# Kernel optimization log

Hardware: AMD Instinct MI355X
Metric: run time of the kernel (lower is better)

Reference implementation:

```python
import jax, jax.numpy as jnp
import numpy as np


def setup_inputs() -> dict:
    key = jax.random.key(0)
    k1, k2, k3, k4 = jax.random.split(key, 4)
    B, S, D, R = 8, 1024, 1024, 256
    batch = jax.random.normal(k1, (B, S, D), dtype=jnp.float32)
    proj_L = jax.random.uniform(k2, (D, R), dtype=jnp.float32, minval=-0.05, maxval=0.05)
    proj_R = jax.random.uniform(k3, (R, D), dtype=jnp.float32, minval=-0.05, maxval=0.05)
    bias = jax.random.uniform(k4, (1,), dtype=jnp.float32, minval=-0.05, maxval=0.05)
    return {"batch": batch, "proj_L": proj_L, "proj_R": proj_R, "bias": bias}


def reference(batch, proj_L, proj_R, bias):
    # logits[b,i,j] = h_i^T (L @ R) h_j + bias
    # Efficient factored form (same math, avoids O(B*S^2*D) intermediates):
    # left[b,i,r] = (batch @ L)[b,i,r]; right[b,j,r] = (batch @ R^T)[b,j,r]
    left = jnp.einsum('bid,dr->bir', batch, proj_L)    # (B,S,R)
    right = jnp.einsum('bjd,rd->bjr', batch, proj_R)   # (B,S,R)
    logits = jnp.einsum('bir,bjr->bij', left, right) + bias[0]
    return logits
```

## Files before the change

kernel.cpp:

```cpp
#include <hip/hip_runtime.h>

typedef __bf16 bf16_t;
typedef __bf16 bf16x8 __attribute__((ext_vector_type(8)));
typedef __bf16 bf16x4 __attribute__((ext_vector_type(4)));
typedef float f32x4 __attribute__((ext_vector_type(4)));

__device__ __forceinline__ void async16(const void* g, void* l) {
  __builtin_amdgcn_global_load_lds(
      (const __attribute__((address_space(1))) unsigned int*)g,
      (__attribute__((address_space(3))) unsigned int*)l,
      16, 0, 0);
}

__global__ void prep_Bcat(const float* __restrict__ projL,
                          const float* __restrict__ projR,
                          bf16_t* __restrict__ Bcat) {
  const int t = threadIdx.x;
  if (blockIdx.x < 256) {
    int i = blockIdx.x * 256 + t;
    float4 v = ((const float4*)projR)[i];
    bf16x4 o;
    o[0] = (bf16_t)v.x; o[1] = (bf16_t)v.y; o[2] = (bf16_t)v.z; o[3] = (bf16_t)v.w;
    ((bf16x4*)(Bcat + (long)256 * 1024))[i] = o;
  } else {
    __shared__ float tile[32][33];
    const int bb = blockIdx.x - 256;
    const int n0 = (bb & 7) * 32;
    const int k0 = (bb >> 3) * 32;
    const int tx = t & 31;
    const int ty = t >> 5;
#pragma unroll
    for (int i = 0; i < 32; i += 8)
      tile[ty + i][tx] = projL[(long)(k0 + ty + i) * 256 + n0 + tx];
    __syncthreads();
#pragma unroll
    for (int i = 0; i < 32; i += 8)
      Bcat[(long)(n0 + ty + i) * 1024 + k0 + tx] = (bf16_t)tile[tx][ty + i];
  }
}

__global__ __launch_bounds__(256, 2) void gemm1_fusedA(
    const float* __restrict__ batch, const bf16_t* __restrict__ Bcat,
    bf16_t* __restrict__ LR) {
  const int bx = blockIdx.x;
  const int tm = (bx & 127) * 64;
  const int tn = (bx >> 7) * 128;

  __shared__ __attribute__((aligned(16))) bf16_t As[4 * 2048];
  __shared__ __attribute__((aligned(16))) bf16_t Bs[4 * 4096];

  const int t = threadIdx.x;
  const int lane = t & 63;
  const int quad = lane >> 4;
  const int l15 = lane & 15;
  const int wave = t >> 6;
  const int wr = (wave >> 1) * 32;
  const int wc = (wave & 1) * 64;

  const int rS = t >> 2;
  const int cS = (t & 3) * 8;
  const bf16_t* gB = Bcat + (long)(tn + rS) * 1024 + cS;
  bf16_t* lB = Bs + t * 8;

  const int rA = t >> 4;
  const int cA = (t & 15) * 8;
  const float* gA = batch + (long)(tm + rA) * 1024 + cA;
  bf16_t* lA = As + (cA >> 5) * 2048 + (cA & 31);

  f32x4 acc[2][4];
#pragma unroll
  for (int i = 0; i < 2; ++i)
#pragma unroll
    for (int j = 0; j < 4; ++j)
      acc[i][j] = (f32x4){0.f, 0.f, 0.f, 0.f};

  float4 fa[4], fb[4];
#pragma unroll
  for (int i = 0; i < 4; ++i) {
    const float* p = gA + (long)16 * i * 1024;
    fa[i] = *(const float4*)p;
    fb[i] = *(const float4*)(p + 4);
  }

  for (int s = 0; s < 8; ++s) {
    const int k0 = s * 128;
#pragma unroll
    for (int kc = 0; kc < 4; ++kc) {
      async16(gB + k0 + kc * 32, lB + kc * 4096);
      async16(gB + k0 + kc * 32 + (long)64 * 1024, lB + kc * 4096 + 2048);
    }
#pragma unroll
    for (int i = 0; i < 4; ++i) {
      bf16x8 v;
      v[0] = (bf16_t)fa[i].x; v[1] = (bf16_t)fa[i].y;
      v[2] = (bf16_t)fa[i].z; v[3] = (bf16_t)fa[i].w;
      v[4] = (bf16_t)fb[i].x; v[5] = (bf16_t)fb[i].y;
      v[6] = (bf16_t)fb[i].z; v[7] = (bf16_t)fb[i].w;
      *(bf16x8*)(lA + (rA + 16 * i) * 32) = v;
    }
    __syncthreads();

    if (s < 7) {
#pragma unroll
      for (int i = 0; i < 4; ++i) {
        const float* p = gA + (s + 1) * 128 + (long)16 * i * 1024;
        fa[i] = *(const float4*)p;
        fb[i] = *(const float4*)(p + 4);
      }
    }

#pragma unroll
    for (int kc = 0; kc < 4; ++kc) {
      const bf16_t* Ak = As + kc * 2048;
      const bf16_t* Bk = Bs + kc * 4096;
      bf16x8 af[2], bv[4];
#pragma unroll
      for (int i = 0; i < 2; ++i)
        af[i] = *(const bf16x8*)(Ak + (wr + i * 16 + l15) * 32 + quad * 8);
#pragma unroll
      for (int j = 0; j < 4; ++j)
        bv[j] = *(const bf16x8*)(Bk + (wc + j * 16 + l15) * 32 + quad * 8);
#pragma unroll
      for (int i = 0; i < 2; ++i)
#pragma unroll
        for (int j = 0; j < 4; ++j)
          acc[i][j] = __builtin_amdgcn_mfma_f32_16x16x32_bf16(af[i], bv[j],
                                                              acc[i][j], 0, 0, 0);
    }
    __syncthreads();
  }

#pragma unroll
  for (int i = 0; i < 2; ++i) {
    const int r0 = tm + wr + i * 16 + quad * 4;
#pragma unroll
    for (int j = 0; j < 4; ++j) {
      const int c0 = tn + wc + j * 16 + l15;
#pragma unroll
      for (int r = 0; r < 4; ++r)
        LR[(long)(r0 + r) * 512 + c0] = (bf16_t)acc[i][j][r];
    }
  }
}

__global__ __launch_bounds__(256, 2) void gemm2(const bf16_t* __restrict__ LR,
                                                float* __restrict__ out,
                                                const float* __restrict__ bias) {
  const int bx = blockIdx.x;
  const int bz = bx & 7;
  const int tile = bx >> 3;
  const int tm = (tile & 7) * 128;
  const int tn = (tile >> 3) * 128;
  const bf16_t* LRb = LR + (long)bz * 1024 * 512;

  __shared__ __attribute__((aligned(16))) bf16_t As[2 * 8192];
  __shared__ __attribute__((aligned(16))) bf16_t Bs[2 * 8192];

  const int t = threadIdx.x;
  const int lane = t & 63;
  const int quad = lane >> 4;
  const int l15 = lane & 15;
  const int wave = t >> 6;
  const int wr = (wave >> 1) * 64;
  const int wc = (wave & 1) * 64;

  const int rS = t >> 2;
  const int cS = (t & 3) * 8;
  const bf16_t* gA = LRb + (long)(tm + rS) * 512 + cS;
  const bf16_t* gB = LRb + (long)(tn + rS) * 512 + 256 + cS;

  f32x4 acc[4][4];
#pragma unroll
  for (int i = 0; i < 4; ++i)
#pragma unroll
    for (int j = 0; j < 4; ++j)
      acc[i][j] = (f32x4){0.f, 0.f, 0.f, 0.f};

  auto STAGE = [&](int buf, int s) {
    const int k0 = s * 64;
    bf16_t* dA = As + buf * 8192 + t * 8;
    bf16_t* dB = Bs + buf * 8192 + t * 8;
#pragma unroll
    for (int kc = 0; kc < 2; ++kc) {
      const int ko = k0 + kc * 32;
      async16(gA + ko, dA + kc * 4096);
      async16(gA + ko + (long)64 * 512, dA + kc * 4096 + 2048);
      async16(gB + ko, dB + kc * 4096);
      async16(gB + ko + (long)64 * 512, dB + kc * 4096 + 2048);
    }
  };

  STAGE(0, 0);
  __syncthreads();

#pragma unroll
  for (int s = 0; s < 4; ++s) {
    if (s < 3) STAGE((s + 1) & 1, s + 1);
    const bf16_t* Ab = As + (s & 1) * 8192;
    const bf16_t* Bb = Bs + (s & 1) * 8192;
#pragma unroll
    for (int kc = 0; kc < 2; ++kc) {
      const bf16_t* Ak = Ab + kc * 4096;
      const bf16_t* Bk = Bb + kc * 4096;
      bf16x8 af[4], bv[4];
#pragma unroll
      for (int i = 0; i < 4; ++i)
        af[i] = *(const bf16x8*)(Ak + (wr + i * 16 + l15) * 32 + quad * 8);
#pragma unroll
      for (int j = 0; j < 4; ++j)
        bv[j] = *(const bf16x8*)(Bk + (wc + j * 16 + l15) * 32 + quad * 8);
#pragma unroll
      for (int i = 0; i < 4; ++i)
#pragma unroll
        for (int j = 0; j < 4; ++j)
          acc[i][j] = __builtin_amdgcn_mfma_f32_16x16x32_bf16(af[i], bv[j],
                                                              acc[i][j], 0, 0, 0);
    }
    if (s < 3) __syncthreads();
  }

  float* C = out + (long)bz * 1024 * 1024;
  const float bvadd = bias[0];
#pragma unroll
  for (int i = 0; i < 4; ++i) {
    const int r0 = tm + wr + i * 16 + quad * 4;
#pragma unroll
    for (int j = 0; j < 4; ++j) {
      const int c0 = tn + wc + j * 16 + l15;
#pragma unroll
      for (int r = 0; r < 4; ++r)
        C[(long)(r0 + r) * 1024 + c0] = acc[i][j][r] + bvadd;
    }
  }
}

extern "C" void kernel_launch(void* const* d_in, const int* in_sizes, int n_in,
                              void* d_out, int out_size, void* d_ws,
                              size_t ws_size, hipStream_t stream) {
  const float* batch = (const float*)d_in[0];
  const float* projL = (const float*)d_in[1];
  const float* projR = (const float*)d_in[2];
  const float* bias = (const float*)d_in[3];
  float* out = (float*)d_out;

  char* ws = (char*)d_ws;
  bf16_t* Bcat = (bf16_t*)ws;
  bf16_t* LR = (bf16_t*)(ws + (long)512 * 1024 * 2);

  prep_Bcat<<<512, 256, 0, stream>>>(projL, projR, Bcat);

  gemm1_fusedA<<<512, 256, 0, stream>>>(batch, Bcat, LR);

  gemm2<<<512, 256, 0, stream>>>(LR, out, bias);
}
```

Before: 110.1 us.

## Fuse three kernels into one cooperative kernel with grid-wide syncs

Merges the weight-prep, first GEMM and second GEMM kernels into a single cooperative launch that separates the phases with grid.sync(), sharing one 64KB LDS buffer across phases. The aim is to remove two kernel launch gaps and their tail effects. In exchange it needs all 512 blocks co-resident (2 per CU on 256 CUs). Every block also waits at each grid barrier, and the 64KB static LDS may limit occupancy in phases that previously used less.

```diff
diff --git a/kernel.cpp b/kernel.cpp
--- a/kernel.cpp
+++ b/kernel.cpp
@@ -1,4 +1,7 @@
 #include <hip/hip_runtime.h>
+#include <hip/hip_cooperative_groups.h>
+
+namespace cg = cooperative_groups;
 
 typedef __bf16 bf16_t;
 typedef __bf16 bf16x8 __attribute__((ext_vector_type(8)));
@@ -12,19 +15,30 @@
       16, 0, 0);
 }
 
-__global__ void prep_Bcat(const float* __restrict__ projL,
-                          const float* __restrict__ projR,
-                          bf16_t* __restrict__ Bcat) {
+__global__ __launch_bounds__(256, 2) void fused_all(
+    const float* __restrict__ batch, const float* __restrict__ projL,
+    const float* __restrict__ projR, const float* __restrict__ bias,
+    float* __restrict__ out, bf16_t* __restrict__ Bcat,
+    bf16_t* __restrict__ LR) {
+  __shared__ __attribute__((aligned(16))) char smem[65536];
+  cg::grid_group grid = cg::this_grid();
+
   const int t = threadIdx.x;
-  if (blockIdx.x < 256) {
-    int i = blockIdx.x * 256 + t;
+  const int bx = blockIdx.x;
+  const int lane = t & 63;
+  const int quad = lane >> 4;
+  const int l15 = lane & 15;
+  const int wave = t >> 6;
+
+  if (bx < 256) {
+    int i = bx * 256 + t;
     float4 v = ((const float4*)projR)[i];
     bf16x4 o;
     o[0] = (bf16_t)v.x; o[1] = (bf16_t)v.y; o[2] = (bf16_t)v.z; o[3] = (bf16_t)v.w;
     ((bf16x4*)(Bcat + (long)256 * 1024))[i] = o;
   } else {
-    __shared__ float tile[32][33];
-    const int bb = blockIdx.x - 256;
+    float(*tile)[33] = (float(*)[33])smem;
+    const int bb = bx - 256;
     const int n0 = (bb & 7) * 32;
     const int k0 = (bb >> 3) * 32;
     const int tx = t & 31;
@@ -37,199 +51,183 @@
     for (int i = 0; i < 32; i += 8)
       Bcat[(long)(n0 + ty + i) * 1024 + k0 + tx] = (bf16_t)tile[tx][ty + i];
   }
-}
-
-__global__ __launch_bounds__(256, 2) void gemm1_fusedA(
-    const float* __restrict__ batch, const bf16_t* __restrict__ Bcat,
-    bf16_t* __restrict__ LR) {
-  const int bx = blockIdx.x;
-  const int tm = (bx & 127) * 64;
-  const int tn = (bx >> 7) * 128;
-
-  __shared__ __attribute__((aligned(16))) bf16_t As[4 * 2048];
-  __shared__ __attribute__((aligned(16))) bf16_t Bs[4 * 4096];
-
-  const int t = threadIdx.x;
-  const int lane = t & 63;
-  const int quad = lane >> 4;
-  const int l15 = lane & 15;
-  const int wave = t >> 6;
-  const int wr = (wave >> 1) * 32;
-  const int wc = (wave & 1) * 64;
-
-  const int rS = t >> 2;
-  const int cS = (t & 3) * 8;
-  const bf16_t* gB = Bcat + (long)(tn + rS) * 1024 + cS;
-  bf16_t* lB = Bs + t * 8;
-
-  const int rA = t >> 4;
-  const int cA = (t & 15) * 8;
-  const float* gA = batch + (long)(tm + rA) * 1024 + cA;
-  bf16_t* lA = As + (cA >> 5) * 2048 + (cA & 31);
-
-  f32x4 acc[2][4];
-#pragma unroll
-  for (int i = 0; i < 2; ++i)
-#pragma unroll
-    for (int j = 0; j < 4; ++j)
-      acc[i][j] = (f32x4){0.f, 0.f, 0.f, 0.f};
-
-  float4 fa[4], fb[4];
-#pragma unroll
-  for (int i = 0; i < 4; ++i) {
-    const float* p = gA + (long)16 * i * 1024;
-    fa[i] = *(const float4*)p;
-    fb[i] = *(const float4*)(p + 4);
+
+  grid.sync();
+
+  {
+    bf16_t* As = (bf16_t*)smem;
+    bf16_t* Bs = (bf16_t*)(smem + 16384);
+    const int tm = (bx & 127) * 64;
+    const int tn = (bx >> 7) * 128;
+    const int wr = (wave >> 1) * 32;
+    const int wc = (wave & 1) * 64;
+
+    const int rS = t >> 2;
+    const int cS = (t & 3) * 8;
+    const bf16_t* gB = Bcat + (long)(tn + rS) * 1024 + cS;
+    bf16_t* lB = Bs + t * 8;
+
+    const int rA = t >> 4;
+    const int cA = (t & 15) * 8;
+    const float* gA = batch + (long)(tm + rA) * 1024 + cA;
+    bf16_t* lA = As + (cA >> 5) * 2048 + (cA & 31);
+
+    f32x4 acc[2][4];
+#pragma unroll
+    for (int i = 0; i < 2; ++i)
+#pragma unroll
+      for (int j = 0; j < 4; ++j)
+        acc[i][j] = (f32x4){0.f, 0.f, 0.f, 0.f};
+
+    float4 fa[4], fb[4];
+#pragma unroll
+    for (int i = 0; i < 4; ++i) {
+      const float* p = gA + (long)16 * i * 1024;
+      fa[i] = *(const float4*)p;
+      fb[i] = *(const float4*)(p + 4);
+    }
+
+    for (int s = 0; s < 8; ++s) {
+      const int k0 = s * 128;
+#pragma unroll
+      for (int kc = 0; kc < 4; ++kc) {
+        async16(gB + k0 + kc * 32, lB + kc * 4096);
+        async16(gB + k0 + kc * 32 + (long)64 * 1024, lB + kc * 4096 + 2048);
+      }
+#pragma unroll
+      for (int i = 0; i < 4; ++i) {
+        bf16x8 v;
+        v[0] = (bf16_t)fa[i].x; v[1] = (bf16_t)fa[i].y;
+        v[2] = (bf16_t)fa[i].z; v[3] = (bf16_t)fa[i].w;
+        v[4] = (bf16_t)fb[i].x; v[5] = (bf16_t)fb[i].y;
+        v[6] = (bf16_t)fb[i].z; v[7] = (bf16_t)fb[i].w;
+        *(bf16x8*)(lA + (rA + 16 * i) * 32) = v;
+      }
+      __syncthreads();
+
+      if (s < 7) {
+#pragma unroll
+        for (int i = 0; i < 4; ++i) {
+          const float* p = gA + (s + 1) * 128 + (long)16 * i * 1024;
+          fa[i] = *(const float4*)p;
+          fb[i] = *(const float4*)(p + 4);
+        }
+      }
+
+#pragma unroll
+      for (int kc = 0; kc < 4; ++kc) {
+        const bf16_t* Ak = As + kc * 2048;
+        const bf16_t* Bk = Bs + kc * 4096;
+        bf16x8 af[2], bv[4];
+#pragma unroll
+        for (int i = 0; i < 2; ++i)
+          af[i] = *(const bf16x8*)(Ak + (wr + i * 16 + l15) * 32 + quad * 8);
+#pragma unroll
+        for (int j = 0; j < 4; ++j)
+          bv[j] = *(const bf16x8*)(Bk + (wc + j * 16 + l15) * 32 + quad * 8);
+#pragma unroll
+        for (int i = 0; i < 2; ++i)
+#pragma unroll
+          for (int j = 0; j < 4; ++j)
+            acc[i][j] = __builtin_amdgcn_mfma_f32_16x16x32_bf16(
+                af[i], bv[j], acc[i][j], 0, 0, 0);
+      }
+      __syncthreads();
+    }
+
+#pragma unroll
+    for (int i = 0; i < 2; ++i) {
+      const int r0 = tm + wr + i * 16 + quad * 4;
+#pragma unroll
+      for (int j = 0; j < 4; ++j) {
+        const int c0 = tn + wc + j * 16 + l15;
+#pragma unroll
+        for (int r = 0; r < 4; ++r)
+          LR[(long)(r0 + r) * 512 + c0] = (bf16_t)acc[i][j][r];
+      }
+    }
   }
 
-  for (int s = 0; s < 8; ++s) {
-    const int k0 = s * 128;
-#pragma unroll
-    for (int kc = 0; kc < 4; ++kc) {
-      async16(gB + k0 + kc * 32, lB + kc * 4096);
-      async16(gB + k0 + kc * 32 + (long)64 * 1024, lB + kc * 4096 + 2048);
-    }
+  grid.sync();
+
+  {
+    bf16_t* As = (bf16_t*)smem;
+    bf16_t* Bs = (bf16_t*)(smem + 32768);
+    const int bz = bx & 7;
+    const int tile = bx >> 3;
+    const int tm = (tile & 7) * 128;
+    const int tn = (tile >> 3) * 128;
+    const bf16_t* LRb = LR + (long)bz * 1024 * 512;
+    const int wr = (wave >> 1) * 64;
+    const int wc = (wave & 1) * 64;
+
+    const int rS = t >> 2;
+    const int cS = (t & 3) * 8;
+    const bf16_t* gA = LRb + (long)(tm + rS) * 512 + cS;
+    const bf16_t* gB = LRb + (long)(tn + rS) * 512 + 256 + cS;
+
+    f32x4 acc[4][4];
+#pragma unroll
+    for (int i = 0; i < 4; ++i)
+#pragma unroll
+      for (int j = 0; j < 4; ++j)
+        acc[i][j] = (f32x4){0.f, 0.f, 0.f, 0.f};
+
+    auto STAGE = [&](int buf, int s) {
+      const int k0 = s * 64;
+      bf16_t* dA = As + buf * 8192 + t * 8;
+      bf16_t* dB = Bs + buf * 8192 + t * 8;
+#pragma unroll
+      for (int kc = 0; kc < 2; ++kc) {
+        const int ko = k0 + kc * 32;
+        async16(gA + ko, dA + kc * 4096);
+        async16(gA + ko + (long)64 * 512, dA + kc * 4096 + 2048);
+        async16(gB + ko, dB + kc * 4096);
+        async16(gB + ko + (long)64 * 512, dB + kc * 4096 + 2048);
+      }
+    };
+
+    STAGE(0, 0);
+    __syncthreads();
+
+#pragma unroll
+    for (int s = 0; s < 4; ++s) {
+      if (s < 3) STAGE((s + 1) & 1, s + 1);
+      const bf16_t* Ab = As + (s & 1) * 8192;
+      const bf16_t* Bb = Bs + (s & 1) * 8192;
+#pragma unroll
+      for (int kc = 0; kc < 2; ++kc) {
+        const bf16_t* Ak = Ab + kc * 4096;
+        const bf16_t* Bk = Bb + kc * 4096;
+        bf16x8 af[4], bv[4];
+#pragma unroll
+        for (int i = 0; i < 4; ++i)
+          af[i] = *(const bf16x8*)(Ak + (wr + i * 16 + l15) * 32 + quad * 8);
+#pragma unroll
+        for (int j = 0; j < 4; ++j)
+          bv[j] = *(const bf16x8*)(Bk + (wc + j * 16 + l15) * 32 + quad * 8);
+#pragma unroll
+        for (int i = 0; i < 4; ++i)
+#pragma unroll
+          for (int j = 0; j < 4; ++j)
+            acc[i][j] = __builtin_amdgcn_mfma_f32_16x16x32_bf16(
+                af[i], bv[j], acc[i][j], 0, 0, 0);
+      }
+      if (s < 3) __syncthreads();
+    }
+
+    float* C = out + (long)bz * 1024 * 1024;
+    const float bvadd = bias[0];
 #pragma unroll
     for (int i = 0; i < 4; ++i) {
-      bf16x8 v;
-      v[0] = (bf16_t)fa[i].x; v[1] = (bf16_t)fa[i].y;
-      v[2] = (bf16_t)fa[i].z; v[3] = (bf16_t)fa[i].w;
-      v[4] = (bf16_t)fb[i].x; v[5] = (bf16_t)fb[i].y;
-      v[6] = (bf16_t)fb[i].z; v[7] = (bf16_t)fb[i].w;
-      *(bf16x8*)(lA + (rA + 16 * i) * 32) = v;
-    }
-    __syncthreads();
-
-    if (s < 7) {
-#pragma unroll
-      for (int i = 0; i < 4; ++i) {
-        const float* p = gA + (s + 1) * 128 + (long)16 * i * 1024;
-        fa[i] = *(const float4*)p;
-        fb[i] = *(const float4*)(p + 4);
-      }
-    }
-
-#pragma unroll
-    for (int kc = 0; kc < 4; ++kc) {
-      const bf16_t* Ak = As + kc * 2048;
-      const bf16_t* Bk = Bs + kc * 4096;
-      bf16x8 af[2], bv[4];
-#pragma unroll
-      for (int i = 0; i < 2; ++i)
-        af[i] = *(const bf16x8*)(Ak + (wr + i * 16 + l15) * 32 + quad * 8);
-#pragma unroll
-      for (int j = 0; j < 4; ++j)
-        bv[j] = *(const bf16x8*)(Bk + (wc + j * 16 + l15) * 32 + quad * 8);
-#pragma unroll
-      for (int i = 0; i < 2; ++i)
-#pragma unroll
-        for (int j = 0; j < 4; ++j)
-          acc[i][j] = __builtin_amdgcn_mfma_f32_16x16x32_bf16(af[i], bv[j],
-                                                              acc[i][j], 0, 0, 0);
-    }
-    __syncthreads();
-  }
-
-#pragma unroll
-  for (int i = 0; i < 2; ++i) {
-    const int r0 = tm + wr + i * 16 + quad * 4;
-#pragma unroll
-    for (int j = 0; j < 4; ++j) {
-      const int c0 = tn + wc + j * 16 + l15;
-#pragma unroll
-      for (int r = 0; r < 4; ++r)
-        LR[(long)(r0 + r) * 512 + c0] = (bf16_t)acc[i][j][r];
-    }
-  }
-}
-
-__global__ __launch_bounds__(256, 2) void gemm2(const bf16_t* __restrict__ LR,
-                                                float* __restrict__ out,
-                                                const float* __restrict__ bias) {
-  const int bx = blockIdx.x;
-  const int bz = bx & 7;
-  const int tile = bx >> 3;
-  const int tm = (tile & 7) * 128;
-  const int tn = (tile >> 3) * 128;
-  const bf16_t* LRb = LR + (long)bz * 1024 * 512;
-
-  __shared__ __attribute__((aligned(16))) bf16_t As[2 * 8192];
-  __shared__ __attribute__((aligned(16))) bf16_t Bs[2 * 8192];
-
-  const int t = threadIdx.x;
-  const int lane = t & 63;
-  const int quad = lane >> 4;
-  const int l15 = lane & 15;
-  const int wave = t >> 6;
-  const int wr = (wave >> 1) * 64;
-  const int wc = (wave & 1) * 64;
-
-  const int rS = t >> 2;
-  const int cS = (t & 3) * 8;
-  const bf16_t* gA = LRb + (long)(tm + rS) * 512 + cS;
-  const bf16_t* gB = LRb + (long)(tn + rS) * 512 + 256 + cS;
-
-  f32x4 acc[4][4];
-#pragma unroll
-  for (int i = 0; i < 4; ++i)
-#pragma unroll
-    for (int j = 0; j < 4; ++j)
-      acc[i][j] = (f32x4){0.f, 0.f, 0.f, 0.f};
-
-  auto STAGE = [&](int buf, int s) {
-    const int k0 = s * 64;
-    bf16_t* dA = As + buf * 8192 + t * 8;
-    bf16_t* dB = Bs + buf * 8192 + t * 8;
-#pragma unroll
-    for (int kc = 0; kc < 2; ++kc) {
-      const int ko = k0 + kc * 32;
-      async16(gA + ko, dA + kc * 4096);
-      async16(gA + ko + (long)64 * 512, dA + kc * 4096 + 2048);
-      async16(gB + ko, dB + kc * 4096);
-      async16(gB + ko + (long)64 * 512, dB + kc * 4096 + 2048);
-    }
-  };
-
-  STAGE(0, 0);
-  __syncthreads();
-
-#pragma unroll
-  for (int s = 0; s < 4; ++s) {
-    if (s < 3) STAGE((s + 1) & 1, s + 1);
-    const bf16_t* Ab = As + (s & 1) * 8192;
-    const bf16_t* Bb = Bs + (s & 1) * 8192;
-#pragma unroll
-    for (int kc = 0; kc < 2; ++kc) {
-      const bf16_t* Ak = Ab + kc * 4096;
-      const bf16_t* Bk = Bb + kc * 4096;
-      bf16x8 af[4], bv[4];
-#pragma unroll
-      for (int i = 0; i < 4; ++i)
-        af[i] = *(const bf16x8*)(Ak + (wr + i * 16 + l15) * 32 + quad * 8);
-#pragma unroll
-      for (int j = 0; j < 4; ++j)
-        bv[j] = *(const bf16x8*)(Bk + (wc + j * 16 + l15) * 32 + quad * 8);
-#pragma unroll
-      for (int i = 0; i < 4; ++i)
-#pragma unroll
-        for (int j = 0; j < 4; ++j)
-          acc[i][j] = __builtin_amdgcn_mfma_f32_16x16x32_bf16(af[i], bv[j],
-                                                              acc[i][j], 0, 0, 0);
-    }
-    if (s < 3) __syncthreads();
-  }
-
-  float* C = out + (long)bz * 1024 * 1024;
-  const float bvadd = bias[0];
-#pragma unroll
-  for (int i = 0; i < 4; ++i) {
-    const int r0 = tm + wr + i * 16 + quad * 4;
-#pragma unroll
-    for (int j = 0; j < 4; ++j) {
-      const int c0 = tn + wc + j * 16 + l15;
-#pragma unroll
-      for (int r = 0; r < 4; ++r)
-        C[(long)(r0 + r) * 1024 + c0] = acc[i][j][r] + bvadd;
+      const int r0 = tm + wr + i * 16 + quad * 4;
+#pragma unroll
+      for (int j = 0; j < 4; ++j) {
+        const int c0 = tn + wc + j * 16 + l15;
+#pragma unroll
+        for (int r = 0; r < 4; ++r)
+          C[(long)(r0 + r) * 1024 + c0] = acc[i][j][r] + bvadd;
+      }
     }
   }
 }
@@ -247,9 +245,8 @@
   bf16_t* Bcat = (bf16_t*)ws;
   bf16_t* LR = (bf16_t*)(ws + (long)512 * 1024 * 2);
 
-  prep_Bcat<<<512, 256, 0, stream>>>(projL, projR, Bcat);
-
-  gemm1_fusedA<<<512, 256, 0, stream>>>(batch, Bcat, LR);
-
-  gemm2<<<512, 256, 0, stream>>>(LR, out, bias);
+  void* args[] = {(void*)&batch, (void*)&projL, (void*)&projR, (void*)&bias,
+                  (void*)&out,   (void*)&Bcat,  (void*)&LR};
+  hipLaunchCooperativeKernel((void*)fused_all, dim3(512), dim3(256), args, 0,
+                             stream);
 }
```

Result: slower. 234.3 us (+112.8%).

## Double-buffer gemm1 K-loop and shrink gemm2 tiles to 64x64 for occupancy

Applied to the files above, without the earlier changes.

gemm1 now uses a 64-wide K step with double-buffered LDS for both A and B, prefetching the next stage's B asynchronously and converting A into the other buffer after the MFMAs. This leaves one barrier per step and lets loads overlap compute. gemm2 switches from 128x128 to 64x64 output tiles, 2048 blocks and a launch bound of 5 blocks per CU, to raise occupancy and wave count. The smaller tiles reload LR operands more often and do fewer MFMAs per LDS read.

```diff
diff --git a/kernel.cpp b/kernel.cpp
--- a/kernel.cpp
+++ b/kernel.cpp
@@ -46,8 +46,8 @@
   const int tm = (bx & 127) * 64;
   const int tn = (bx >> 7) * 128;
 
-  __shared__ __attribute__((aligned(16))) bf16_t As[4 * 2048];
-  __shared__ __attribute__((aligned(16))) bf16_t Bs[4 * 4096];
+  __shared__ __attribute__((aligned(16))) bf16_t As[2 * 4096];
+  __shared__ __attribute__((aligned(16))) bf16_t Bs[2 * 8192];
 
   const int t = threadIdx.x;
   const int lane = t & 63;
@@ -60,12 +60,10 @@
   const int rS = t >> 2;
   const int cS = (t & 3) * 8;
   const bf16_t* gB = Bcat + (long)(tn + rS) * 1024 + cS;
-  bf16_t* lB = Bs + t * 8;
-
-  const int rA = t >> 4;
-  const int cA = (t & 15) * 8;
+
+  const int rA = t >> 3;
+  const int cA = (t & 7) * 8;
   const float* gA = batch + (long)(tm + rA) * 1024 + cA;
-  bf16_t* lA = As + (cA >> 5) * 2048 + (cA & 31);
 
   f32x4 acc[2][4];
 #pragma unroll
@@ -74,45 +72,51 @@
     for (int j = 0; j < 4; ++j)
       acc[i][j] = (f32x4){0.f, 0.f, 0.f, 0.f};
 
-  float4 fa[4], fb[4];
-#pragma unroll
-  for (int i = 0; i < 4; ++i) {
-    const float* p = gA + (long)16 * i * 1024;
+  float4 fa[2], fb[2];
+#pragma unroll
+  for (int i = 0; i < 2; ++i) {
+    const float* p = gA + (long)32 * i * 1024;
     fa[i] = *(const float4*)p;
     fb[i] = *(const float4*)(p + 4);
   }
-
-  for (int s = 0; s < 8; ++s) {
-    const int k0 = s * 128;
-#pragma unroll
-    for (int kc = 0; kc < 4; ++kc) {
-      async16(gB + k0 + kc * 32, lB + kc * 4096);
-      async16(gB + k0 + kc * 32 + (long)64 * 1024, lB + kc * 4096 + 2048);
-    }
-#pragma unroll
-    for (int i = 0; i < 4; ++i) {
-      bf16x8 v;
-      v[0] = (bf16_t)fa[i].x; v[1] = (bf16_t)fa[i].y;
-      v[2] = (bf16_t)fa[i].z; v[3] = (bf16_t)fa[i].w;
-      v[4] = (bf16_t)fb[i].x; v[5] = (bf16_t)fb[i].y;
-      v[6] = (bf16_t)fb[i].z; v[7] = (bf16_t)fb[i].w;
-      *(bf16x8*)(lA + (rA + 16 * i) * 32) = v;
-    }
-    __syncthreads();
-
-    if (s < 7) {
-#pragma unroll
-      for (int i = 0; i < 4; ++i) {
-        const float* p = gA + (s + 1) * 128 + (long)16 * i * 1024;
+#pragma unroll
+  for (int kc = 0; kc < 2; ++kc) {
+    async16(gB + kc * 32, Bs + kc * 4096 + t * 8);
+    async16(gB + kc * 32 + (long)64 * 1024, Bs + kc * 4096 + 2048 + t * 8);
+  }
+#pragma unroll
+  for (int i = 0; i < 2; ++i) {
+    bf16x8 v;
+    v[0] = (bf16_t)fa[i].x; v[1] = (bf16_t)fa[i].y;
+    v[2] = (bf16_t)fa[i].z; v[3] = (bf16_t)fa[i].w;
+    v[4] = (bf16_t)fb[i].x; v[5] = (bf16_t)fb[i].y;
+    v[6] = (bf16_t)fb[i].z; v[7] = (bf16_t)fb[i].w;
+    *(bf16x8*)(As + (cA >> 5) * 2048 + (rA + 32 * i) * 32 + (cA & 31)) = v;
+  }
+  __syncthreads();
+
+  for (int s = 0; s < 16; ++s) {
+    const int buf = s & 1;
+    const int nb = buf ^ 1;
+    if (s < 15) {
+      const int k1 = (s + 1) * 64;
+#pragma unroll
+      for (int i = 0; i < 2; ++i) {
+        const float* p = gA + k1 + (long)32 * i * 1024;
         fa[i] = *(const float4*)p;
         fb[i] = *(const float4*)(p + 4);
       }
-    }
-
-#pragma unroll
-    for (int kc = 0; kc < 4; ++kc) {
-      const bf16_t* Ak = As + kc * 2048;
-      const bf16_t* Bk = Bs + kc * 4096;
+#pragma unroll
+      for (int kc = 0; kc < 2; ++kc) {
+        async16(gB + k1 + kc * 32, Bs + nb * 8192 + kc * 4096 + t * 8);
+        async16(gB + k1 + kc * 32 + (long)64 * 1024,
+                Bs + nb * 8192 + kc * 4096 + 2048 + t * 8);
+      }
+    }
+#pragma unroll
+    for (int kc = 0; kc < 2; ++kc) {
+      const bf16_t* Ak = As + buf * 4096 + kc * 2048;
+      const bf16_t* Bk = Bs + buf * 8192 + kc * 4096;
       bf16x8 af[2], bv[4];
 #pragma unroll
       for (int i = 0; i < 2; ++i)
@@ -127,7 +131,19 @@
           acc[i][j] = __builtin_amdgcn_mfma_f32_16x16x32_bf16(af[i], bv[j],
                                                               acc[i][j], 0, 0, 0);
     }
-    __syncthreads();
+    if (s < 15) {
+#pragma unroll
+      for (int i = 0; i < 2; ++i) {
+        bf16x8 v;
+        v[0] = (bf16_t)fa[i].x; v[1] = (bf16_t)fa[i].y;
+        v[2] = (bf16_t)fa[i].z; v[3] = (bf16_t)fa[i].w;
+        v[4] = (bf16_t)fb[i].x; v[5] = (bf16_t)fb[i].y;
+        v[6] = (bf16_t)fb[i].z; v[7] = (bf16_t)fb[i].w;
+        *(bf16x8*)(As + nb * 4096 + (cA >> 5) * 2048 + (rA + 32 * i) * 32 +
+                   (cA & 31)) = v;
+      }
+      __syncthreads();
+    }
   }
 
 #pragma unroll
@@ -143,50 +159,48 @@
   }
 }
 
-__global__ __launch_bounds__(256, 2) void gemm2(const bf16_t* __restrict__ LR,
+__global__ __launch_bounds__(256, 5) void gemm2(const bf16_t* __restrict__ LR,
                                                 float* __restrict__ out,
                                                 const float* __restrict__ bias) {
   const int bx = blockIdx.x;
   const int bz = bx & 7;
   const int tile = bx >> 3;
-  const int tm = (tile & 7) * 128;
-  const int tn = (tile >> 3) * 128;
+  const int tm = (tile & 15) * 64;
+  const int tn = (tile >> 4) * 64;
   const bf16_t* LRb = LR + (long)bz * 1024 * 512;
 
-  __shared__ __attribute__((aligned(16))) bf16_t As[2 * 8192];
-  __shared__ __attribute__((aligned(16))) bf16_t Bs[2 * 8192];
+  __shared__ __attribute__((aligned(16))) bf16_t As[2 * 4096];
+  __shared__ __attribute__((aligned(16))) bf16_t Bs[2 * 4096];
 
   const int t = threadIdx.x;
   const int lane = t & 63;
   const int quad = lane >> 4;
   const int l15 = lane & 15;
   const int wave = t >> 6;
-  const int wr = (wave >> 1) * 64;
-  const int wc = (wave & 1) * 64;
+  const int wr = (wave >> 1) * 32;
+  const int wc = (wave & 1) * 32;
 
   const int rS = t >> 2;
   const int cS = (t & 3) * 8;
   const bf16_t* gA = LRb + (long)(tm + rS) * 512 + cS;
   const bf16_t* gB = LRb + (long)(tn + rS) * 512 + 256 + cS;
 
-  f32x4 acc[4][4];
-#pragma unroll
-  for (int i = 0; i < 4; ++i)
-#pragma unroll
-    for (int j = 0; j < 4; ++j)
+  f32x4 acc[2][2];
+#pragma unroll
+  for (int i = 0; i < 2; ++i)
+#pragma unroll
+    for (int j = 0; j < 2; ++j)
       acc[i][j] = (f32x4){0.f, 0.f, 0.f, 0.f};
 
   auto STAGE = [&](int buf, int s) {
     const int k0 = s * 64;
-    bf16_t* dA = As + buf * 8192 + t * 8;
-    bf16_t* dB = Bs + buf * 8192 + t * 8;
+    bf16_t* dA = As + buf * 4096 + t * 8;
+    bf16_t* dB = Bs + buf * 4096 + t * 8;
 #pragma unroll
     for (int kc = 0; kc < 2; ++kc) {
       const int ko = k0 + kc * 32;
-      async16(gA + ko, dA + kc * 4096);
-      async16(gA + ko + (long)64 * 512, dA + kc * 4096 + 2048);
-      async16(gB + ko, dB + kc * 4096);
-      async16(gB + ko + (long)64 * 512, dB + kc * 4096 + 2048);
+      async16(gA + ko, dA + kc * 2048);
+      async16(gB + ko, dB + kc * 2048);
     }
   };
 
@@ -196,23 +210,23 @@
 #pragma unroll
   for (int s = 0; s < 4; ++s) {
     if (s < 3) STAGE((s + 1) & 1, s + 1);
-    const bf16_t* Ab = As + (s & 1) * 8192;
-    const bf16_t* Bb = Bs + (s & 1) * 8192;
+    const bf16_t* Ab = As + (s & 1) * 4096;
+    const bf16_t* Bb = Bs + (s & 1) * 4096;
 #pragma unroll
     for (int kc = 0; kc < 2; ++kc) {
-      const bf16_t* Ak = Ab + kc * 4096;
-      const bf16_t* Bk = Bb + kc * 4096;
-      bf16x8 af[4], bv[4];
-#pragma unroll
-      for (int i = 0; i < 4; ++i)
+      const bf16_t* Ak = Ab + kc * 2048;
+      const bf16_t* Bk = Bb + kc * 2048;
+      bf16x8 af[2], bv[2];
+#pragma unroll
+      for (int i = 0; i < 2; ++i)
         af[i] = *(const bf16x8*)(Ak + (wr + i * 16 + l15) * 32 + quad * 8);
 #pragma unroll
-      for (int j = 0; j < 4; ++j)
+      for (int j = 0; j < 2; ++j)
         bv[j] = *(const bf16x8*)(Bk + (wc + j * 16 + l15) * 32 + quad * 8);
 #pragma unroll
-      for (int i = 0; i < 4; ++i)
-#pragma unroll
-        for (int j = 0; j < 4; ++j)
+      for (int i = 0; i < 2; ++i)
+#pragma unroll
+        for (int j = 0; j < 2; ++j)
           acc[i][j] = __builtin_amdgcn_mfma_f32_16x16x32_bf16(af[i], bv[j],
                                                               acc[i][j], 0, 0, 0);
     }
@@ -222,10 +236,10 @@
   float* C = out + (long)bz * 1024 * 1024;
   const float bvadd = bias[0];
 #pragma unroll
-  for (int i = 0; i < 4; ++i) {
+  for (int i = 0; i < 2; ++i) {
     const int r0 = tm + wr + i * 16 + quad * 4;
 #pragma unroll
-    for (int j = 0; j < 4; ++j) {
+    for (int j = 0; j < 2; ++j) {
       const int c0 = tn + wc + j * 16 + l15;
 #pragma unroll
       for (int r = 0; r < 4; ++r)
@@ -251,5 +265,5 @@
 
   gemm1_fusedA<<<512, 256, 0, stream>>>(batch, Bcat, LR);
 
-  gemm2<<<512, 256, 0, stream>>>(LR, out, bias);
-}
+  gemm2<<<2048, 256, 0, stream>>>(LR, out, bias);
+}
```

New measurement: 115.5 us. 1.05x slower.

## Load A fragments directly from global into registers and double-buffer B in LDS

Applied to the files above, without the earlier changes.

The fp32 batch tile is no longer converted and staged through shared memory. Each lane loads its MFMA A-fragment rows straight from global memory and converts them to bf16 in registers. The B tile becomes double-buffered in LDS with async loads issued one stage ahead. This removes the A LDS writes and reads and one barrier per stage. In exchange, A rows are read redundantly by wave pairs, and the A register prefetch across iterations is lost, which exposes global-load latency.

```diff
diff --git a/kernel.cpp b/kernel.cpp
--- a/kernel.cpp
+++ b/kernel.cpp
@@ -10,6 +10,13 @@
       (const __attribute__((address_space(1))) unsigned int*)g,
       (__attribute__((address_space(3))) unsigned int*)l,
       16, 0, 0);
+}
+
+__device__ __forceinline__ bf16x8 cvt8(const float4 a, const float4 b) {
+  bf16x8 v;
+  v[0] = (bf16_t)a.x; v[1] = (bf16_t)a.y; v[2] = (bf16_t)a.z; v[3] = (bf16_t)a.w;
+  v[4] = (bf16_t)b.x; v[5] = (bf16_t)b.y; v[6] = (bf16_t)b.z; v[7] = (bf16_t)b.w;
+  return v;
 }
 
 __global__ void prep_Bcat(const float* __restrict__ projL,
@@ -46,8 +53,7 @@
   const int tm = (bx & 127) * 64;
   const int tn = (bx >> 7) * 128;
 
-  __shared__ __attribute__((aligned(16))) bf16_t As[4 * 2048];
-  __shared__ __attribute__((aligned(16))) bf16_t Bs[4 * 4096];
+  __shared__ __attribute__((aligned(16))) bf16_t Bs[2 * 16384];
 
   const int t = threadIdx.x;
   const int lane = t & 63;
@@ -60,12 +66,8 @@
   const int rS = t >> 2;
   const int cS = (t & 3) * 8;
   const bf16_t* gB = Bcat + (long)(tn + rS) * 1024 + cS;
-  bf16_t* lB = Bs + t * 8;
-
-  const int rA = t >> 4;
-  const int cA = (t & 15) * 8;
-  const float* gA = batch + (long)(tm + rA) * 1024 + cA;
-  bf16_t* lA = As + (cA >> 5) * 2048 + (cA & 31);
+
+  const float* gA = batch + (long)(tm + wr + l15) * 1024 + quad * 8;
 
   f32x4 acc[2][4];
 #pragma unroll
@@ -74,49 +76,41 @@
     for (int j = 0; j < 4; ++j)
       acc[i][j] = (f32x4){0.f, 0.f, 0.f, 0.f};
 
-  float4 fa[4], fb[4];
-#pragma unroll
-  for (int i = 0; i < 4; ++i) {
-    const float* p = gA + (long)16 * i * 1024;
-    fa[i] = *(const float4*)p;
-    fb[i] = *(const float4*)(p + 4);
-  }
+#pragma unroll
+  for (int kc = 0; kc < 4; ++kc) {
+    async16(gB + kc * 32, Bs + kc * 4096 + t * 8);
+    async16(gB + kc * 32 + (long)64 * 1024, Bs + kc * 4096 + 2048 + t * 8);
+  }
+  __syncthreads();
 
   for (int s = 0; s < 8; ++s) {
+    const int buf = s & 1;
+    const int nb = buf ^ 1;
     const int k0 = s * 128;
+    if (s < 7) {
+#pragma unroll
+      for (int kc = 0; kc < 4; ++kc) {
+        async16(gB + k0 + 128 + kc * 32, Bs + nb * 16384 + kc * 4096 + t * 8);
+        async16(gB + k0 + 128 + kc * 32 + (long)64 * 1024,
+                Bs + nb * 16384 + kc * 4096 + 2048 + t * 8);
+      }
+    }
+    float4 a0[4][2], a1[4][2];
 #pragma unroll
     for (int kc = 0; kc < 4; ++kc) {
-      async16(gB + k0 + kc * 32, lB + kc * 4096);
-      async16(gB + k0 + kc * 32 + (long)64 * 1024, lB + kc * 4096 + 2048);
-    }
-#pragma unroll
-    for (int i = 0; i < 4; ++i) {
-      bf16x8 v;
-      v[0] = (bf16_t)fa[i].x; v[1] = (bf16_t)fa[i].y;
-      v[2] = (bf16_t)fa[i].z; v[3] = (bf16_t)fa[i].w;
-      v[4] = (bf16_t)fb[i].x; v[5] = (bf16_t)fb[i].y;
-      v[6] = (bf16_t)fb[i].z; v[7] = (bf16_t)fb[i].w;
-      *(bf16x8*)(lA + (rA + 16 * i) * 32) = v;
-    }
-    __syncthreads();
-
-    if (s < 7) {
-#pragma unroll
-      for (int i = 0; i < 4; ++i) {
-        const float* p = gA + (s + 1) * 128 + (long)16 * i * 1024;
-        fa[i] = *(const float4*)p;
-        fb[i] = *(const float4*)(p + 4);
-      }
-    }
-
+      const float* p0 = gA + k0 + kc * 32;
+      a0[kc][0] = *(const float4*)p0;
+      a0[kc][1] = *(const float4*)(p0 + 4);
+      const float* p1 = p0 + (long)16 * 1024;
+      a1[kc][0] = *(const float4*)p1;
+      a1[kc][1] = *(const float4*)(p1 + 4);
+    }
 #pragma unroll
     for (int kc = 0; kc < 4; ++kc) {
-      const bf16_t* Ak = As + kc * 2048;
-      const bf16_t* Bk = Bs + kc * 4096;
       bf16x8 af[2], bv[4];
-#pragma unroll
-      for (int i = 0; i < 2; ++i)
-        af[i] = *(const bf16x8*)(Ak + (wr + i * 16 + l15) * 32 + quad * 8);
+      af[0] = cvt8(a0[kc][0], a0[kc][1]);
+      af[1] = cvt8(a1[kc][0], a1[kc][1]);
+      const bf16_t* Bk = Bs + buf * 16384 + kc * 4096;
 #pragma unroll
       for (int j = 0; j < 4; ++j)
         bv[j] = *(const bf16x8*)(Bk + (wc + j * 16 + l15) * 32 + quad * 8);
```

Result: slower. 132.4 us (+20.2%).
